# Kernel optimization log

Hardware: AMD Instinct MI355X
Metric: run time of the kernel (lower is better)

## Reference

```python
import jax, jax.numpy as jnp
import numpy as np
import math

B, T, D = 2, 2048, 2048
H, KV, HD = 16, 4, 128  # n_heads, n_kv_heads, head_dim
ROPE_BASE = 10000.0


def setup_inputs() -> dict:
    key = jax.random.key(0)
    ks = jax.random.split(key, 5)
    s = 0.02
    return {
        "x": jax.random.normal(ks[0], (B, T, D), dtype=jnp.float32),
        "Wq": jax.random.normal(ks[1], (D, H * HD), dtype=jnp.float32) * s,
        "Wk": jax.random.normal(ks[2], (D, KV * HD), dtype=jnp.float32) * s,
        "Wv": jax.random.normal(ks[3], (D, KV * HD), dtype=jnp.float32) * s,
        "Wo": jax.random.normal(ks[4], (H * HD, D), dtype=jnp.float32) * s,
    }


def _rope_tables(t_len, dtype):
    inv_freq = 1.0 / (ROPE_BASE ** (jnp.arange(0, HD, 2, dtype=jnp.float32) / HD))
    t = jnp.arange(t_len, dtype=jnp.float32)
    freqs = t[:, None] * inv_freq[None, :]  # [T, HD/2]
    return jnp.cos(freqs).astype(dtype), jnp.sin(freqs).astype(dtype)


def _apply_rope(x, cos, sin):
    # x: [B, h, T, HD]; cos/sin: [T, HD/2] broadcast to [1,1,T,HD/2]
    c = cos[None, None, :, :]
    s = sin[None, None, :, :]
    x1, x2 = x[..., ::2], x[..., 1::2]
    rot = jnp.stack([x1 * c - x2 * s, x1 * s + x2 * c], axis=-1)  # interleave back
    return rot.reshape(x.shape)


def reference(x, Wq, Wk, Wv, Wo):
    b, t, d = x.shape
    q = (x @ Wq).reshape(b, t, H, HD).transpose(0, 2, 1, 3)   # [B,H,T,HD]
    k = (x @ Wk).reshape(b, t, KV, HD).transpose(0, 2, 1, 3)  # [B,KV,T,HD]
    v = (x @ Wv).reshape(b, t, KV, HD).transpose(0, 2, 1, 3)

    cos, sin = _rope_tables(t, x.dtype)
    q = _apply_rope(q, cos, sin)
    k = _apply_rope(k, cos, sin)

    rep = H // KV
    k_rep = jnp.repeat(k, rep, axis=1)  # [B,H,T,HD]
    v_rep = jnp.repeat(v, rep, axis=1)

    scale = 1.0 / math.sqrt(HD)
    scores = jnp.einsum("bhqd,bhkd->bhqk", q, k_rep) * scale
    causal = jnp.triu(jnp.ones((t, t), dtype=bool), k=1)
    neg = jnp.finfo(scores.dtype).min
    scores = jnp.where(causal[None, None, :, :], neg, scores)
    attn = jax.nn.softmax(scores, axis=-1)
    out = jnp.einsum("bhqk,bhkd->bhqd", attn, v_rep)
    y = out.transpose(0, 2, 1, 3).reshape(b, t, H * HD) @ Wo
    return y
```

## Files before the change

### kernel.cpp

```cpp
#include <hip/hip_runtime.h>
#include <cstdint>
#include <math.h>

#define T_SEQ 2048
#define BATCH 2
#define NH 16
#define NKV 4
#define HD 128

typedef __attribute__((ext_vector_type(8))) short short8;
typedef __attribute__((ext_vector_type(4))) float f32x4;

__device__ __forceinline__ ushort f2bf(float f) {
  uint32_t u = __builtin_bit_cast(uint32_t, f);
  u += 0x7FFF + ((u >> 16) & 1);
  return (ushort)(u >> 16);
}
__device__ __forceinline__ float bf2f(ushort u) {
  uint32_t v = ((uint32_t)u) << 16;
  return __builtin_bit_cast(float, v);
}
__device__ __forceinline__ void ld16(void* lds, const void* g) {
  __builtin_amdgcn_global_load_lds((const __attribute__((address_space(1))) void*)g,
                                   (__attribute__((address_space(3))) void*)lds,
                                   16, 0, 0);
}

__global__ __launch_bounds__(256) void convert_f32_bf16(const float* __restrict__ in,
                                                        ushort* __restrict__ out, int n) {
  int i = (blockIdx.x * 256 + threadIdx.x) * 4;
  if (i >= n) return;
  float4 v = *(const float4*)&in[i];
  ushort4 o;
  o.x = f2bf(v.x); o.y = f2bf(v.y); o.z = f2bf(v.z); o.w = f2bf(v.w);
  *(ushort4*)&out[i] = o;
}

__global__ __launch_bounds__(256) void transpose_f32_bf16(const float* __restrict__ in,
                                                          ushort* __restrict__ out,
                                                          int K, int N) {
  __shared__ float tile[32][33];
  int n0 = blockIdx.x * 32, k0 = blockIdx.y * 32;
  int r = threadIdx.x >> 3, c4 = (threadIdx.x & 7) << 2;
  float4 v = *(const float4*)&in[(size_t)(k0 + r) * N + n0 + c4];
  tile[r][c4 + 0] = v.x; tile[r][c4 + 1] = v.y;
  tile[r][c4 + 2] = v.z; tile[r][c4 + 3] = v.w;
  __syncthreads();
  ushort4 o;
  o.x = f2bf(tile[c4 + 0][r]); o.y = f2bf(tile[c4 + 1][r]);
  o.z = f2bf(tile[c4 + 2][r]); o.w = f2bf(tile[c4 + 3][r]);
  *(ushort4*)&out[(size_t)(n0 + r) * K + k0 + c4] = o;
}

template <typename OutT>
__global__ __launch_bounds__(256) void gemm_bt(const ushort* __restrict__ A,
                                               const ushort* __restrict__ Bt,
                                               OutT* __restrict__ C,
                                               int M, int N, int K) {
  __shared__ __align__(16) ushort As[128 * 32];
  __shared__ __align__(16) ushort Bs[128 * 32];
  const int tid = threadIdx.x;
  const int w = tid >> 6, l = tid & 63;
  const int wr = w >> 1, wc = w & 1;
  const int quad = l >> 4, l15 = l & 15;
  const int bm = blockIdx.y * 128, bn = blockIdx.x * 128;

  f32x4 acc[4][4];
#pragma unroll
  for (int mi = 0; mi < 4; ++mi)
#pragma unroll
    for (int ni = 0; ni < 4; ++ni)
#pragma unroll
      for (int r = 0; r < 4; ++r) acc[mi][ni][r] = 0.f;

  for (int k0 = 0; k0 < K; k0 += 32) {
    __syncthreads();
#pragma unroll
    for (int j = 0; j < 2; ++j) {
      int r0 = w * 32 + j * 16;
      int row = r0 + (l >> 2);
      int gc = (l & 3) ^ ((row >> 1) & 3);
      ld16(&As[r0 * 32], &A[(size_t)(bm + row) * K + k0 + gc * 8]);
      ld16(&Bs[r0 * 32], &Bt[(size_t)(bn + row) * K + k0 + gc * 8]);
    }
    __syncthreads();
    short8 af[4], bf[4];
#pragma unroll
    for (int mi = 0; mi < 4; ++mi) {
      int m = wr * 64 + mi * 16 + l15;
      af[mi] = *(const short8*)&As[m * 32 + (quad ^ ((m >> 1) & 3)) * 8];
    }
#pragma unroll
    for (int ni = 0; ni < 4; ++ni) {
      int n = wc * 64 + ni * 16 + l15;
      bf[ni] = *(const short8*)&Bs[n * 32 + (quad ^ ((n >> 1) & 3)) * 8];
    }
#pragma unroll
    for (int mi = 0; mi < 4; ++mi)
#pragma unroll
      for (int ni = 0; ni < 4; ++ni)
        acc[mi][ni] = __builtin_amdgcn_mfma_f32_16x16x32_bf16(af[mi], bf[ni], acc[mi][ni], 0, 0, 0);
  }
#pragma unroll
  for (int mi = 0; mi < 4; ++mi)
#pragma unroll
    for (int ni = 0; ni < 4; ++ni)
#pragma unroll
      for (int r = 0; r < 4; ++r) {
        int grow = bm + wr * 64 + mi * 16 + quad * 4 + r;
        int gcol = bn + wc * 64 + ni * 16 + l15;
        if constexpr (__is_same(OutT, ushort))
          C[(size_t)grow * N + gcol] = f2bf(acc[mi][ni][r]);
        else
          C[(size_t)grow * N + gcol] = acc[mi][ni][r];
      }
}

__global__ __launch_bounds__(256) void rope_k_bf16(ushort* __restrict__ qkv) {
  int idx = blockIdx.x * 256 + threadIdx.x;
  const int PAIRS_PER_ROW = 256;
  if (idx >= BATCH * T_SEQ * PAIRS_PER_ROW) return;
  int row = idx >> 8;
  int kp = idx & 255;
  int t = row & (T_SEQ - 1);
  int i = kp & 63;
  ushort* ptr = qkv + (size_t)row * 3072 + 2048 + 2 * kp;
  float inv = expf((float)i * -0.14391156831212788f);
  float ang = (float)t * inv;
  float sn, cs;
  sincosf(ang, &sn, &cs);
  float x1 = bf2f(ptr[0]), x2 = bf2f(ptr[1]);
  ptr[0] = f2bf(x1 * cs - x2 * sn);
  ptr[1] = f2bf(x1 * sn + x2 * cs);
}

__global__ __launch_bounds__(256) void transpose_v(const ushort* __restrict__ qkv,
                                                   ushort* __restrict__ vT) {
  __shared__ ushort tile[32][34];
  int m0 = blockIdx.x * 32, d0 = blockIdx.y * 32;
  int r = threadIdx.x >> 3, c4 = (threadIdx.x & 7) << 2;
  ushort4 v = *(const ushort4*)&qkv[(size_t)(m0 + r) * 3072 + 2560 + d0 + c4];
  tile[r][c4 + 0] = v.x; tile[r][c4 + 1] = v.y;
  tile[r][c4 + 2] = v.z; tile[r][c4 + 3] = v.w;
  __syncthreads();
  ushort4 o;
  o.x = tile[c4 + 0][r]; o.y = tile[c4 + 1][r];
  o.z = tile[c4 + 2][r]; o.w = tile[c4 + 3][r];
  *(ushort4*)&vT[(size_t)(d0 + r) * 4096 + m0 + c4] = o;
}

__global__ __launch_bounds__(256, 2) void attn_mfma(const ushort* __restrict__ qkv,
                                                    const ushort* __restrict__ vT,
                                                    ushort* __restrict__ ao) {
  __shared__ __align__(16) ushort Ks[2][64 * 128];
  __shared__ __align__(16) ushort Vt[2][128 * 64];
  __shared__ __align__(16) ushort Ps[4][16 * 64];
  const int tid = threadIdx.x;
  const int w = tid >> 6, l = tid & 63;
  const int quad = l >> 4, l15 = l & 15;
  const int qt0 = (gridDim.x - 1 - blockIdx.x) * 64;
  const int h = blockIdx.y, b = blockIdx.z;
  const int kvh = h >> 2;
  const size_t qrow0 = (size_t)b * T_SEQ + qt0;
  const size_t krow0 = (size_t)b * T_SEQ;
  const float SC = 0.12751744595764253f;

  const int t_pos = qt0 + w * 16 + l15;
  short8 qf[4];
#pragma unroll
  for (int kc = 0; kc < 4; ++kc) {
    short8 raw = *(const short8*)&qkv[(qrow0 + w * 16 + l15) * 3072 + h * 128 + kc * 32 + quad * 8];
#pragma unroll
    for (int u = 0; u < 4; ++u) {
      int i_idx = kc * 16 + quad * 4 + u;
      float inv = expf((float)i_idx * -0.14391156831212788f);
      float ang = (float)t_pos * inv;
      float sn, cs;
      sincosf(ang, &sn, &cs);
      float x1 = bf2f((ushort)raw[2 * u]);
      float x2 = bf2f((ushort)raw[2 * u + 1]);
      qf[kc][2 * u]     = (short)f2bf(x1 * cs - x2 * sn);
      qf[kc][2 * u + 1] = (short)f2bf(x1 * sn + x2 * cs);
    }
  }

  f32x4 oacc[8];
#pragma unroll
  for (int i = 0; i < 8; ++i)
#pragma unroll
    for (int r = 0; r < 4; ++r) oacc[i][r] = 0.f;
  float lpart[4] = {0.f, 0.f, 0.f, 0.f};

  ushort* pw = Ps[w];
  const int within = l & 7;
  const int colbase = l15 >> 3;

  auto stage = [&](int kt, int bufi) {
    const int kt0 = kt << 6;
    ushort* kb = Ks[bufi];
    ushort* vb = Vt[bufi];
#pragma unroll
    for (int j = 0; j < 4; ++j) {
      int r0 = w * 16 + j * 4;
      int row = r0 + (l >> 4);
      int gc = (l & 15) ^ ((row >> 1) & 7);
      ld16(&kb[r0 * 128], &qkv[(krow0 + kt0 + row) * 3072 + 2048 + kvh * 128 + gc * 8]);
    }
#pragma unroll
    for (int j = 0; j < 4; ++j) {
      int r0 = w * 32 + j * 8;
      int row = r0 + (l >> 3);
      int gc = (l & 7) ^ (row & 7);
      ld16(&vb[r0 * 64], &vT[(size_t)(kvh * 128 + row) * 4096 + krow0 + kt0 + gc * 8]);
    }
  };

  const int nkt = (qt0 >> 6) + 1;
  stage(0, 0);
  for (int kt = 0; kt < nkt; ++kt) {
    __syncthreads();
    if (kt + 1 < nkt) stage(kt + 1, (kt + 1) & 1);
    const ushort* kb = Ks[kt & 1];
    const ushort* vb = Vt[kt & 1];

    f32x4 sacc[4];
#pragma unroll
    for (int ni = 0; ni < 4; ++ni)
#pragma unroll
      for (int r = 0; r < 4; ++r) sacc[ni][r] = 0.f;
#pragma unroll
    for (int kc = 0; kc < 4; ++kc) {
#pragma unroll
      for (int ni = 0; ni < 4; ++ni) {
        int n = ni * 16 + l15;
        short8 bfr = *(const short8*)&kb[n * 128 + ((kc * 4 + quad) ^ ((n >> 1) & 7)) * 8];
        sacc[ni] = __builtin_amdgcn_mfma_f32_16x16x32_bf16(qf[kc], bfr, sacc[ni], 0, 0, 0);
      }
    }

    if (kt == nkt - 1) {
      const int rowbase = w * 16 + quad * 4;
#pragma unroll
      for (int ni = 0; ni < 4; ++ni) {
        const int colid = ni * 16 + l15;
#pragma unroll
        for (int r = 0; r < 4; ++r) {
          float s = (colid > rowbase + r) ? -1e30f : sacc[ni][r] * SC;
          float pv = __builtin_amdgcn_exp2f(s);
          lpart[r] += pv;
          int prow = quad * 4 + r;
          pw[prow * 64 + (((ni * 2 + colbase) ^ (prow & 7)) << 3) + within] = f2bf(pv);
        }
      }
    } else {
#pragma unroll
      for (int ni = 0; ni < 4; ++ni)
#pragma unroll
        for (int r = 0; r < 4; ++r) {
          float pv = __builtin_amdgcn_exp2f(sacc[ni][r] * SC);
          lpart[r] += pv;
          int prow = quad * 4 + r;
          pw[prow * 64 + (((ni * 2 + colbase) ^ (prow & 7)) << 3) + within] = f2bf(pv);
        }
    }

#pragma unroll
    for (int kc = 0; kc < 2; ++kc) {
      short8 a = *(const short8*)&pw[l15 * 64 + ((kc * 4 + quad) ^ (l15 & 7)) * 8];
#pragma unroll
      for (int ni2 = 0; ni2 < 8; ++ni2) {
        int d = ni2 * 16 + l15;
        short8 bfr = *(const short8*)&vb[d * 64 + ((kc * 4 + quad) ^ (d & 7)) * 8];
        oacc[ni2] = __builtin_amdgcn_mfma_f32_16x16x32_bf16(a, bfr, oacc[ni2], 0, 0, 0);
      }
    }
  }

#pragma unroll
  for (int r = 0; r < 4; ++r) {
    float lv = lpart[r];
    lv += __shfl_xor(lv, 1);
    lv += __shfl_xor(lv, 2);
    lv += __shfl_xor(lv, 4);
    lv += __shfl_xor(lv, 8);
    float inv = 1.f / lv;
    size_t grow = qrow0 + w * 16 + quad * 4 + r;
#pragma unroll
    for (int ni2 = 0; ni2 < 8; ++ni2)
      ao[grow * 2048 + h * 128 + ni2 * 16 + l15] = f2bf(oacc[ni2][r] * inv);
  }
}

extern "C" void kernel_launch(void* const* d_in, const int* in_sizes, int n_in,
                              void* d_out, int out_size, void* d_ws, size_t ws_size,
                              hipStream_t stream) {
  const float* x  = (const float*)d_in[0];
  const float* Wq = (const float*)d_in[1];
  const float* Wk = (const float*)d_in[2];
  const float* Wv = (const float*)d_in[3];
  const float* Wo = (const float*)d_in[4];
  float* y = (float*)d_out;

  const int M = BATCH * T_SEQ;
  ushort* xb    = (ushort*)d_ws;
  ushort* wqkvT = xb + (size_t)M * 2048;
  ushort* woT   = wqkvT + (size_t)3072 * 2048;
  ushort* qkv   = woT + (size_t)2048 * 2048;
  ushort* vTb   = qkv + (size_t)M * 3072;
  ushort* aob   = vTb + (size_t)512 * 4096;

  dim3 blk(256);
  convert_f32_bf16<<<(M * 2048 / 4 + 255) / 256, blk, 0, stream>>>(x, xb, M * 2048);
  transpose_f32_bf16<<<dim3(64, 64), blk, 0, stream>>>(Wq, wqkvT, 2048, 2048);
  transpose_f32_bf16<<<dim3(16, 64), blk, 0, stream>>>(Wk, wqkvT + (size_t)2048 * 2048, 2048, 512);
  transpose_f32_bf16<<<dim3(16, 64), blk, 0, stream>>>(Wv, wqkvT + (size_t)2560 * 2048, 2048, 512);
  transpose_f32_bf16<<<dim3(64, 64), blk, 0, stream>>>(Wo, woT, 2048, 2048);

  gemm_bt<ushort><<<dim3(3072 / 128, M / 128), blk, 0, stream>>>(xb, wqkvT, qkv, M, 3072, 2048);

  rope_k_bf16<<<(M * 256 + 255) / 256, blk, 0, stream>>>(qkv);
  transpose_v<<<dim3(M / 32, 512 / 32), blk, 0, stream>>>(qkv, vTb);

  attn_mfma<<<dim3(T_SEQ / 64, NH, BATCH), blk, 0, stream>>>(qkv, vTb, aob);

  gemm_bt<float><<<dim3(2048 / 128, M / 128), blk, 0, stream>>>(aob, woT, y, M, 2048, 2048);
}
```

Before: 367.4 us.

## Fuse prep kernels, fold RoPE/V-transpose into QKV GEMM epilogue, GQA-shared attention blocks

Merges the x conversion and the four weight transposes into one prep launch. Applies K RoPE and the V transpose inside the QKV GEMM epilogue, removing two separate passes over qkv. Restructures attention so each 512-thread block serves all four query heads of one KV head, sharing K/V tiles, with 32-row query tiles paired as (63-i, i) to balance causal work. It also folds the softmax scale into Q and truncates P to bf16 instead of rounding it, which reduces precision slightly.

```diff
diff --git a/kernel.cpp b/kernel.cpp
--- a/kernel.cpp
+++ b/kernel.cpp
@@ -16,6 +16,9 @@
   u += 0x7FFF + ((u >> 16) & 1);
   return (ushort)(u >> 16);
 }
+__device__ __forceinline__ ushort f2bf_trunc(float f) {
+  return (ushort)(__builtin_bit_cast(uint32_t, f) >> 16);
+}
 __device__ __forceinline__ float bf2f(ushort u) {
   uint32_t v = ((uint32_t)u) << 16;
   return __builtin_bit_cast(float, v);
@@ -26,22 +29,33 @@
                                    16, 0, 0);
 }
 
-__global__ __launch_bounds__(256) void convert_f32_bf16(const float* __restrict__ in,
-                                                        ushort* __restrict__ out, int n) {
-  int i = (blockIdx.x * 256 + threadIdx.x) * 4;
-  if (i >= n) return;
-  float4 v = *(const float4*)&in[i];
-  ushort4 o;
-  o.x = f2bf(v.x); o.y = f2bf(v.y); o.z = f2bf(v.z); o.w = f2bf(v.w);
-  *(ushort4*)&out[i] = o;
-}
-
-__global__ __launch_bounds__(256) void transpose_f32_bf16(const float* __restrict__ in,
-                                                          ushort* __restrict__ out,
-                                                          int K, int N) {
+__global__ __launch_bounds__(256) void prep(
+    const float* __restrict__ x, ushort* __restrict__ xb,
+    const float* __restrict__ Wq, const float* __restrict__ Wk,
+    const float* __restrict__ Wv, const float* __restrict__ Wo,
+    ushort* __restrict__ wqkvT, ushort* __restrict__ woT) {
   __shared__ float tile[32][33];
-  int n0 = blockIdx.x * 32, k0 = blockIdx.y * 32;
-  int r = threadIdx.x >> 3, c4 = (threadIdx.x & 7) << 2;
+  const int bid = blockIdx.x;
+  const int tid = threadIdx.x;
+  if (bid < 8192) {
+    int i = (bid * 256 + tid) * 4;
+    float4 v = *(const float4*)&x[i];
+    ushort4 o;
+    o.x = f2bf(v.x); o.y = f2bf(v.y); o.z = f2bf(v.z); o.w = f2bf(v.w);
+    *(ushort4*)&xb[i] = o;
+    return;
+  }
+  const float* in;
+  ushort* out;
+  int N, lid;
+  if (bid < 12288)      { in = Wq; out = wqkvT;                        N = 2048; lid = bid - 8192; }
+  else if (bid < 13312) { in = Wk; out = wqkvT + (size_t)2048 * 2048;  N = 512;  lid = bid - 12288; }
+  else if (bid < 14336) { in = Wv; out = wqkvT + (size_t)2560 * 2048;  N = 512;  lid = bid - 13312; }
+  else                  { in = Wo; out = woT;                          N = 2048; lid = bid - 14336; }
+  const int K = 2048;
+  const int nb = N / 32;
+  const int n0 = (lid % nb) * 32, k0 = (lid / nb) * 32;
+  const int r = tid >> 3, c4 = (tid & 7) << 2;
   float4 v = *(const float4*)&in[(size_t)(k0 + r) * N + n0 + c4];
   tile[r][c4 + 0] = v.x; tile[r][c4 + 1] = v.y;
   tile[r][c4 + 2] = v.z; tile[r][c4 + 3] = v.w;
@@ -52,10 +66,12 @@
   *(ushort4*)&out[(size_t)(n0 + r) * K + k0 + c4] = o;
 }
 
-template <typename OutT>
+template <int MODE>
 __global__ __launch_bounds__(256) void gemm_bt(const ushort* __restrict__ A,
                                                const ushort* __restrict__ Bt,
-                                               OutT* __restrict__ C,
+                                               float* __restrict__ Cf,
+                                               ushort* __restrict__ Cq,
+                                               ushort* __restrict__ vTo,
                                                int M, int N, int K) {
   __shared__ __align__(16) ushort As[128 * 32];
   __shared__ __align__(16) ushort Bs[128 * 32];
@@ -101,95 +117,81 @@
       for (int ni = 0; ni < 4; ++ni)
         acc[mi][ni] = __builtin_amdgcn_mfma_f32_16x16x32_bf16(af[mi], bf[ni], acc[mi][ni], 0, 0, 0);
   }
-#pragma unroll
-  for (int mi = 0; mi < 4; ++mi)
-#pragma unroll
-    for (int ni = 0; ni < 4; ++ni)
-#pragma unroll
-      for (int r = 0; r < 4; ++r) {
-        int grow = bm + wr * 64 + mi * 16 + quad * 4 + r;
-        int gcol = bn + wc * 64 + ni * 16 + l15;
-        if constexpr (__is_same(OutT, ushort))
-          C[(size_t)grow * N + gcol] = f2bf(acc[mi][ni][r]);
-        else
-          C[(size_t)grow * N + gcol] = acc[mi][ni][r];
-      }
-}
-
-__global__ __launch_bounds__(256) void rope_k_bf16(ushort* __restrict__ qkv) {
-  int idx = blockIdx.x * 256 + threadIdx.x;
-  const int PAIRS_PER_ROW = 256;
-  if (idx >= BATCH * T_SEQ * PAIRS_PER_ROW) return;
-  int row = idx >> 8;
-  int kp = idx & 255;
-  int t = row & (T_SEQ - 1);
-  int i = kp & 63;
-  ushort* ptr = qkv + (size_t)row * 3072 + 2048 + 2 * kp;
-  float inv = expf((float)i * -0.14391156831212788f);
-  float ang = (float)t * inv;
-  float sn, cs;
-  sincosf(ang, &sn, &cs);
-  float x1 = bf2f(ptr[0]), x2 = bf2f(ptr[1]);
-  ptr[0] = f2bf(x1 * cs - x2 * sn);
-  ptr[1] = f2bf(x1 * sn + x2 * cs);
-}
-
-__global__ __launch_bounds__(256) void transpose_v(const ushort* __restrict__ qkv,
-                                                   ushort* __restrict__ vT) {
-  __shared__ ushort tile[32][34];
-  int m0 = blockIdx.x * 32, d0 = blockIdx.y * 32;
-  int r = threadIdx.x >> 3, c4 = (threadIdx.x & 7) << 2;
-  ushort4 v = *(const ushort4*)&qkv[(size_t)(m0 + r) * 3072 + 2560 + d0 + c4];
-  tile[r][c4 + 0] = v.x; tile[r][c4 + 1] = v.y;
-  tile[r][c4 + 2] = v.z; tile[r][c4 + 3] = v.w;
-  __syncthreads();
-  ushort4 o;
-  o.x = tile[c4 + 0][r]; o.y = tile[c4 + 1][r];
-  o.z = tile[c4 + 2][r]; o.w = tile[c4 + 3][r];
-  *(ushort4*)&vT[(size_t)(d0 + r) * 4096 + m0 + c4] = o;
-}
-
-__global__ __launch_bounds__(256, 2) void attn_mfma(const ushort* __restrict__ qkv,
+  if constexpr (MODE == 0) {
+#pragma unroll
+    for (int mi = 0; mi < 4; ++mi)
+#pragma unroll
+      for (int ni = 0; ni < 4; ++ni)
+#pragma unroll
+        for (int r = 0; r < 4; ++r) {
+          int grow = bm + wr * 64 + mi * 16 + quad * 4 + r;
+          int gcol = bn + wc * 64 + ni * 16 + l15;
+          Cf[(size_t)grow * N + gcol] = acc[mi][ni][r];
+        }
+  } else {
+    const int sec = bn >> 7;
+    if (sec < 16) {
+#pragma unroll
+      for (int mi = 0; mi < 4; ++mi)
+#pragma unroll
+        for (int ni = 0; ni < 4; ++ni)
+#pragma unroll
+          for (int r = 0; r < 4; ++r) {
+            int grow = bm + wr * 64 + mi * 16 + quad * 4 + r;
+            int gcol = bn + wc * 64 + ni * 16 + l15;
+            Cq[(size_t)grow * 3072 + gcol] = f2bf(acc[mi][ni][r]);
+          }
+    } else if (sec < 20) {
+#pragma unroll
+      for (int mi = 0; mi < 4; ++mi)
+#pragma unroll
+        for (int ni = 0; ni < 4; ++ni) {
+          int gcol = bn + wc * 64 + ni * 16 + l15;
+          int pos = gcol & 127;
+          float inv = expf((float)(pos >> 1) * -0.14391156831212788f);
+#pragma unroll
+          for (int r = 0; r < 4; ++r) {
+            float val = acc[mi][ni][r];
+            float part = __shfl_xor(val, 1);
+            int grow = bm + wr * 64 + mi * 16 + quad * 4 + r;
+            float sn, cs;
+            sincosf((float)(grow & (T_SEQ - 1)) * inv, &sn, &cs);
+            float o = (pos & 1) ? (part * sn + val * cs) : (val * cs - part * sn);
+            Cq[(size_t)grow * 3072 + gcol] = f2bf(o);
+          }
+        }
+    } else {
+#pragma unroll
+      for (int mi = 0; mi < 4; ++mi)
+#pragma unroll
+        for (int ni = 0; ni < 4; ++ni) {
+          int d = bn - 2560 + wc * 64 + ni * 16 + l15;
+          int grow0 = bm + wr * 64 + mi * 16 + quad * 4;
+          ushort4 o4;
+          o4.x = f2bf(acc[mi][ni][0]);
+          o4.y = f2bf(acc[mi][ni][1]);
+          o4.z = f2bf(acc[mi][ni][2]);
+          o4.w = f2bf(acc[mi][ni][3]);
+          *(ushort4*)&vTo[(size_t)d * 4096 + grow0] = o4;
+        }
+    }
+  }
+}
+
+__global__ __launch_bounds__(512, 2) void attn_mfma(const ushort* __restrict__ qkv,
                                                     const ushort* __restrict__ vT,
                                                     ushort* __restrict__ ao) {
   __shared__ __align__(16) ushort Ks[2][64 * 128];
   __shared__ __align__(16) ushort Vt[2][128 * 64];
-  __shared__ __align__(16) ushort Ps[4][16 * 64];
+  __shared__ __align__(16) ushort Ps[8][16 * 64];
   const int tid = threadIdx.x;
   const int w = tid >> 6, l = tid & 63;
   const int quad = l >> 4, l15 = l & 15;
-  const int qt0 = (gridDim.x - 1 - blockIdx.x) * 64;
-  const int h = blockIdx.y, b = blockIdx.z;
-  const int kvh = h >> 2;
-  const size_t qrow0 = (size_t)b * T_SEQ + qt0;
+  const int hw = w >> 1, sub = w & 1;
+  const int kvh = blockIdx.y, b = blockIdx.z;
+  const int h = kvh * 4 + hw;
   const size_t krow0 = (size_t)b * T_SEQ;
   const float SC = 0.12751744595764253f;
-
-  const int t_pos = qt0 + w * 16 + l15;
-  short8 qf[4];
-#pragma unroll
-  for (int kc = 0; kc < 4; ++kc) {
-    short8 raw = *(const short8*)&qkv[(qrow0 + w * 16 + l15) * 3072 + h * 128 + kc * 32 + quad * 8];
-#pragma unroll
-    for (int u = 0; u < 4; ++u) {
-      int i_idx = kc * 16 + quad * 4 + u;
-      float inv = expf((float)i_idx * -0.14391156831212788f);
-      float ang = (float)t_pos * inv;
-      float sn, cs;
-      sincosf(ang, &sn, &cs);
-      float x1 = bf2f((ushort)raw[2 * u]);
-      float x2 = bf2f((ushort)raw[2 * u + 1]);
-      qf[kc][2 * u]     = (short)f2bf(x1 * cs - x2 * sn);
-      qf[kc][2 * u + 1] = (short)f2bf(x1 * sn + x2 * cs);
-    }
-  }
-
-  f32x4 oacc[8];
-#pragma unroll
-  for (int i = 0; i < 8; ++i)
-#pragma unroll
-    for (int r = 0; r < 4; ++r) oacc[i][r] = 0.f;
-  float lpart[4] = {0.f, 0.f, 0.f, 0.f};
 
   ushort* pw = Ps[w];
   const int within = l & 7;
@@ -200,94 +202,129 @@
     ushort* kb = Ks[bufi];
     ushort* vb = Vt[bufi];
 #pragma unroll
-    for (int j = 0; j < 4; ++j) {
-      int r0 = w * 16 + j * 4;
+    for (int j = 0; j < 2; ++j) {
+      int r0 = w * 8 + j * 4;
       int row = r0 + (l >> 4);
       int gc = (l & 15) ^ ((row >> 1) & 7);
       ld16(&kb[r0 * 128], &qkv[(krow0 + kt0 + row) * 3072 + 2048 + kvh * 128 + gc * 8]);
     }
 #pragma unroll
-    for (int j = 0; j < 4; ++j) {
-      int r0 = w * 32 + j * 8;
+    for (int j = 0; j < 2; ++j) {
+      int r0 = w * 16 + j * 8;
       int row = r0 + (l >> 3);
       int gc = (l & 7) ^ (row & 7);
       ld16(&vb[r0 * 64], &vT[(size_t)(kvh * 128 + row) * 4096 + krow0 + kt0 + gc * 8]);
     }
   };
 
-  const int nkt = (qt0 >> 6) + 1;
-  stage(0, 0);
-  for (int kt = 0; kt < nkt; ++kt) {
+#pragma unroll 1
+  for (int ph = 0; ph < 2; ++ph) {
+    const int qt = ph ? (int)blockIdx.x : 63 - (int)blockIdx.x;
+    const int qt0 = qt << 5;
+    const size_t qrow0 = krow0 + qt0;
+
+    const int t_pos = qt0 + sub * 16 + l15;
+    short8 qf[4];
+#pragma unroll
+    for (int kc = 0; kc < 4; ++kc) {
+      short8 raw = *(const short8*)&qkv[(qrow0 + sub * 16 + l15) * 3072 + h * 128 + kc * 32 + quad * 8];
+#pragma unroll
+      for (int u = 0; u < 4; ++u) {
+        int i_idx = kc * 16 + quad * 4 + u;
+        float inv = expf((float)i_idx * -0.14391156831212788f);
+        float sn, cs;
+        sincosf((float)t_pos * inv, &sn, &cs);
+        cs *= SC; sn *= SC;
+        float x1 = bf2f((ushort)raw[2 * u]);
+        float x2 = bf2f((ushort)raw[2 * u + 1]);
+        qf[kc][2 * u]     = (short)f2bf(x1 * cs - x2 * sn);
+        qf[kc][2 * u + 1] = (short)f2bf(x1 * sn + x2 * cs);
+      }
+    }
+
+    f32x4 oacc[8];
+#pragma unroll
+    for (int i = 0; i < 8; ++i)
+#pragma unroll
+      for (int r = 0; r < 4; ++r) oacc[i][r] = 0.f;
+    float lpart[4] = {0.f, 0.f, 0.f, 0.f};
+
+    const int nkt = (qt >> 1) + 1;
     __syncthreads();
-    if (kt + 1 < nkt) stage(kt + 1, (kt + 1) & 1);
-    const ushort* kb = Ks[kt & 1];
-    const ushort* vb = Vt[kt & 1];
-
-    f32x4 sacc[4];
-#pragma unroll
-    for (int ni = 0; ni < 4; ++ni)
-#pragma unroll
-      for (int r = 0; r < 4; ++r) sacc[ni][r] = 0.f;
-#pragma unroll
-    for (int kc = 0; kc < 4; ++kc) {
-#pragma unroll
-      for (int ni = 0; ni < 4; ++ni) {
-        int n = ni * 16 + l15;
-        short8 bfr = *(const short8*)&kb[n * 128 + ((kc * 4 + quad) ^ ((n >> 1) & 7)) * 8];
-        sacc[ni] = __builtin_amdgcn_mfma_f32_16x16x32_bf16(qf[kc], bfr, sacc[ni], 0, 0, 0);
+    stage(0, 0);
+    for (int kt = 0; kt < nkt; ++kt) {
+      __syncthreads();
+      if (kt + 1 < nkt) stage(kt + 1, (kt + 1) & 1);
+      const ushort* kb = Ks[kt & 1];
+      const ushort* vb = Vt[kt & 1];
+
+      f32x4 sacc[4];
+#pragma unroll
+      for (int ni = 0; ni < 4; ++ni)
+#pragma unroll
+        for (int r = 0; r < 4; ++r) sacc[ni][r] = 0.f;
+#pragma unroll
+      for (int kc = 0; kc < 4; ++kc) {
+#pragma unroll
+        for (int ni = 0; ni < 4; ++ni) {
+          int n = ni * 16 + l15;
+          short8 bfr = *(const short8*)&kb[n * 128 + ((kc * 4 + quad) ^ ((n >> 1) & 7)) * 8];
+          sacc[ni] = __builtin_amdgcn_mfma_f32_16x16x32_bf16(qf[kc], bfr, sacc[ni], 0, 0, 0);
+        }
       }
-    }
-
-    if (kt == nkt - 1) {
-      const int rowbase = w * 16 + quad * 4;
-#pragma unroll
-      for (int ni = 0; ni < 4; ++ni) {
-        const int colid = ni * 16 + l15;
-#pragma unroll
-        for (int r = 0; r < 4; ++r) {
-          float s = (colid > rowbase + r) ? -1e30f : sacc[ni][r] * SC;
-          float pv = __builtin_amdgcn_exp2f(s);
-          lpart[r] += pv;
-          int prow = quad * 4 + r;
-          pw[prow * 64 + (((ni * 2 + colbase) ^ (prow & 7)) << 3) + within] = f2bf(pv);
-        }
+
+      const int kt0 = kt << 6;
+      if (kt == nkt - 1) {
+        const int rowg = qt0 + sub * 16 + quad * 4;
+#pragma unroll
+        for (int ni = 0; ni < 4; ++ni) {
+          const int colid = kt0 + ni * 16 + l15;
+#pragma unroll
+          for (int r = 0; r < 4; ++r) {
+            float s = (colid > rowg + r) ? -1e30f : sacc[ni][r];
+            float pv = __builtin_amdgcn_exp2f(s);
+            lpart[r] += pv;
+            int prow = quad * 4 + r;
+            pw[prow * 64 + (((ni * 2 + colbase) ^ (prow & 7)) << 3) + within] = f2bf_trunc(pv);
+          }
+        }
+      } else {
+#pragma unroll
+        for (int ni = 0; ni < 4; ++ni)
+#pragma unroll
+          for (int r = 0; r < 4; ++r) {
+            float pv = __builtin_amdgcn_exp2f(sacc[ni][r]);
+            lpart[r] += pv;
+            int prow = quad * 4 + r;
+            pw[prow * 64 + (((ni * 2 + colbase) ^ (prow & 7)) << 3) + within] = f2bf_trunc(pv);
+          }
       }
-    } else {
-#pragma unroll
-      for (int ni = 0; ni < 4; ++ni)
-#pragma unroll
-        for (int r = 0; r < 4; ++r) {
-          float pv = __builtin_amdgcn_exp2f(sacc[ni][r] * SC);
-          lpart[r] += pv;
-          int prow = quad * 4 + r;
-          pw[prow * 64 + (((ni * 2 + colbase) ^ (prow & 7)) << 3) + within] = f2bf(pv);
-        }
-    }
-
-#pragma unroll
-    for (int kc = 0; kc < 2; ++kc) {
-      short8 a = *(const short8*)&pw[l15 * 64 + ((kc * 4 + quad) ^ (l15 & 7)) * 8];
-#pragma unroll
-      for (int ni2 = 0; ni2 < 8; ++ni2) {
-        int d = ni2 * 16 + l15;
-        short8 bfr = *(const short8*)&vb[d * 64 + ((kc * 4 + quad) ^ (d & 7)) * 8];
-        oacc[ni2] = __builtin_amdgcn_mfma_f32_16x16x32_bf16(a, bfr, oacc[ni2], 0, 0, 0);
+
+#pragma unroll
+      for (int kc = 0; kc < 2; ++kc) {
+        short8 a = *(const short8*)&pw[l15 * 64 + ((kc * 4 + quad) ^ (l15 & 7)) * 8];
+#pragma unroll
+        for (int ni2 = 0; ni2 < 8; ++ni2) {
+          int d = ni2 * 16 + l15;
+          short8 bfr = *(const short8*)&vb[d * 64 + ((kc * 4 + quad) ^ (d & 7)) * 8];
+          oacc[ni2] = __builtin_amdgcn_mfma_f32_16x16x32_bf16(a, bfr, oacc[ni2], 0, 0, 0);
+        }
       }
     }
-  }
-
-#pragma unroll
-  for (int r = 0; r < 4; ++r) {
-    float lv = lpart[r];
-    lv += __shfl_xor(lv, 1);
-    lv += __shfl_xor(lv, 2);
-    lv += __shfl_xor(lv, 4);
-    lv += __shfl_xor(lv, 8);
-    float inv = 1.f / lv;
-    size_t grow = qrow0 + w * 16 + quad * 4 + r;
-#pragma unroll
-    for (int ni2 = 0; ni2 < 8; ++ni2)
-      ao[grow * 2048 + h * 128 + ni2 * 16 + l15] = f2bf(oacc[ni2][r] * inv);
+
+#pragma unroll
+    for (int r = 0; r < 4; ++r) {
+      float lv = lpart[r];
+      lv += __shfl_xor(lv, 1);
+      lv += __shfl_xor(lv, 2);
+      lv += __shfl_xor(lv, 4);
+      lv += __shfl_xor(lv, 8);
+      float inv = 1.f / lv;
+      size_t grow = qrow0 + sub * 16 + quad * 4 + r;
+#pragma unroll
+      for (int ni2 = 0; ni2 < 8; ++ni2)
+        ao[grow * 2048 + h * 128 + ni2 * 16 + l15] = f2bf(oacc[ni2][r] * inv);
+    }
   }
 }
 
@@ -309,19 +346,13 @@
   ushort* vTb   = qkv + (size_t)M * 3072;
   ushort* aob   = vTb + (size_t)512 * 4096;
 
-  dim3 blk(256);
-  convert_f32_bf16<<<(M * 2048 / 4 + 255) / 256, blk, 0, stream>>>(x, xb, M * 2048);
-  transpose_f32_bf16<<<dim3(64, 64), blk, 0, stream>>>(Wq, wqkvT, 2048, 2048);
-  transpose_f32_bf16<<<dim3(16, 64), blk, 0, stream>>>(Wk, wqkvT + (size_t)2048 * 2048, 2048, 512);
-  transpose_f32_bf16<<<dim3(16, 64), blk, 0, stream>>>(Wv, wqkvT + (size_t)2560 * 2048, 2048, 512);
-  transpose_f32_bf16<<<dim3(64, 64), blk, 0, stream>>>(Wo, woT, 2048, 2048);
-
-  gemm_bt<ushort><<<dim3(3072 / 128, M / 128), blk, 0, stream>>>(xb, wqkvT, qkv, M, 3072, 2048);
-
-  rope_k_bf16<<<(M * 256 + 255) / 256, blk, 0, stream>>>(qkv);
-  transpose_v<<<dim3(M / 32, 512 / 32), blk, 0, stream>>>(qkv, vTb);
-
-  attn_mfma<<<dim3(T_SEQ / 64, NH, BATCH), blk, 0, stream>>>(qkv, vTb, aob);
-
-  gemm_bt<float><<<dim3(2048 / 128, M / 128), blk, 0, stream>>>(aob, woT, y, M, 2048, 2048);
-}
+  prep<<<18432, 256, 0, stream>>>(x, xb, Wq, Wk, Wv, Wo, wqkvT, woT);
+
+  gemm_bt<1><<<dim3(3072 / 128, M / 128), 256, 0, stream>>>(
+      xb, wqkvT, nullptr, qkv, vTb, M, 3072, 2048);
+
+  attn_mfma<<<dim3(32, NKV, BATCH), 512, 0, stream>>>(qkv, vTb, aob);
+
+  gemm_bt<0><<<dim3(2048 / 128, M / 128), 256, 0, stream>>>(
+      aob, woT, y, nullptr, nullptr, M, 2048, 2048);
+}
```

After: 948.0 us. +158.0%, slower.
